# Kernel tuning notes

Measured on AMD Instinct MI355X. Metric: run time of the kernel, lower is better.

## Reference

```python
import jax, jax.numpy as jnp
import numpy as np

N_NODES = 10000
N_EDGES = 160000


def setup_inputs() -> dict:
    key = jax.random.key(0)
    ks = jax.random.split(key, 8)
    B, S, N, C, H, E = 2, 32, N_NODES, 1, 32, N_EDGES
    x = jax.random.normal(ks[0], (B, S, N, C), dtype=jnp.float32)
    mask = jax.random.randint(ks[1], (B, S, N, C), 0, 2) > 0  # True = observed
    edge_index = jax.random.randint(ks[2], (2, E), 0, N, dtype=jnp.int32)
    edge_weight = jax.random.uniform(ks[3], (E,), dtype=jnp.float32)
    W1 = jax.random.normal(ks[4], (C, H), dtype=jnp.float32) * (1.0 / np.sqrt(C))
    b1 = jnp.zeros((H,), dtype=jnp.float32)
    W2 = jax.random.normal(ks[5], (H, C), dtype=jnp.float32) * (1.0 / np.sqrt(H))
    b2 = jnp.zeros((C,), dtype=jnp.float32)
    return {"x": x, "mask": mask, "edge_index": edge_index,
            "edge_weight": edge_weight, "W1": W1, "b1": b1, "W2": W2, "b2": b2}


def _gcn_norm(edge_index, edge_weight, num_nodes, dtype):
    # PyG gcn_norm: add self-loops (weight 1), symmetric D^-1/2 A D^-1/2.
    src, dst = edge_index[0], edge_index[1]
    loop = jnp.arange(num_nodes, dtype=edge_index.dtype)
    src = jnp.concatenate([src, loop])
    dst = jnp.concatenate([dst, loop])
    w = jnp.concatenate([edge_weight, jnp.ones((num_nodes,), dtype)])
    deg = jax.ops.segment_sum(w, dst, num_segments=num_nodes)
    dinv = jnp.where(deg > 0, jax.lax.rsqrt(deg), 0.0)
    norm = dinv[src] * w * dinv[dst]  # (E + N,)
    return src, dst, norm


def _gcn_layer(h, W, b, src, dst, norm, num_nodes):
    # h: (G, N, Fin) batched over G = B*S replicas sharing one graph.
    h = h @ W                                        # (G, N, Fout)
    msg = norm[None, :, None] * h[:, src, :]         # (G, E+N, Fout)
    agg = jnp.zeros((h.shape[0], num_nodes, W.shape[1]), h.dtype)
    agg = agg.at[:, dst, :].add(msg)
    return agg + b


def reference(x, mask, edge_index, edge_weight, W1, b1, W2, b2):
    B, S, N, C = x.shape
    src, dst, norm = _gcn_norm(edge_index, edge_weight, N, x.dtype)
    h = x.reshape(B * S, N, C)  # fuse per-(batch,step) loop into one batched pass
    h = jax.nn.relu(_gcn_layer(h, W1, b1, src, dst, norm, N))
    h = _gcn_layer(h, W2, b2, src, dst, norm, N)
    out = h.reshape(B, S, N, C)
    # impute_only_holes at eval time: keep observed values
    out = jnp.where(mask, x, out)
    return out
```

## Files before the change

### kernel.cpp

```cpp
#include <hip/hip_runtime.h>


#define G   64
#define CAP 64
#define POISON   0xAAAAAAAAu
#define DEG_INV  1.52587890625e-5f

__global__ void k1_prep(const float* __restrict__ x,
                        const int* __restrict__ src, const int* __restrict__ dst,
                        const float* __restrict__ ew,
                        unsigned* __restrict__ packed,
                        int2* __restrict__ bucket, float* __restrict__ xt,
                        int N, int E, int ntile) {
    if ((int)blockIdx.x < ntile) {
        __shared__ float tile[64][65];
        int n0 = blockIdx.x * 64;
        int lane = threadIdx.x & 63, wq = threadIdx.x >> 6;
#pragma unroll
        for (int i = 0; i < 16; ++i) {
            int g = wq + i * 4;
            int n = n0 + lane;
            if (n < N) tile[g][lane] = x[(size_t)g * N + n];
        }
        __syncthreads();
#pragma unroll
        for (int i = 0; i < 16; ++i) {
            int nl = wq + i * 4;
            int n = n0 + nl;
            if (n < N) xt[(size_t)n * G + lane] = tile[lane][nl];
        }
    } else {
        int e = (blockIdx.x - ntile) * blockDim.x + threadIdx.x;
        if (e < E) {
            int d = dst[e], s = src[e];
            float w = ew[e];
            unsigned add = (1u << 24) + (unsigned)__float2uint_rn(w * 65536.0f);
            unsigned pos = (atomicAdd(&packed[d], add) >> 24) - 0xAAu;
            if (pos < CAP) bucket[(size_t)d * CAP + pos] = make_int2(s, __float_as_int(w));
        }
    }
}

__device__ __forceinline__ float di_of(unsigned hdr) {
    return rsqrtf((float)(hdr & 0xFFFFFFu) * DEG_INV + 1.0f);
}

__global__ void k2_gather_phi(const int2* __restrict__ bucket,
                              const unsigned* __restrict__ packed,
                              const float* __restrict__ xt,
                              const float* __restrict__ W1,
                              const float* __restrict__ b1,
                              const float* __restrict__ W2,
                              float* __restrict__ zt, int N) {
    int d    = (blockIdx.x * blockDim.x + threadIdx.x) >> 6;
    int lane = threadIdx.x & 63;
    if (d >= N) return;
    unsigned hdr = packed[d] - POISON;
    int kn = (int)(hdr >> 24); if (kn > CAP) kn = CAP;
    float di = di_of(hdr);
    size_t base = (size_t)d * CAP;
    const int4* b4 = (const int4*)(bucket + base);
    float sacc = 0.0f;
    int k = 0;
    for (; k + 4 <= kn; k += 4) {
        int4 pA = b4[k >> 1];
        int4 pB = b4[(k >> 1) + 1];
        float f0 = xt[(size_t)pA.x * G + lane];
        float f1 = xt[(size_t)pA.z * G + lane];
        float f2 = xt[(size_t)pB.x * G + lane];
        float f3 = xt[(size_t)pB.z * G + lane];
        unsigned h0 = packed[pA.x] - POISON;
        unsigned h1 = packed[pA.z] - POISON;
        unsigned h2 = packed[pB.x] - POISON;
        unsigned h3 = packed[pB.z] - POISON;
        sacc = fmaf(__int_as_float(pA.y) * di_of(h0), f0, sacc);
        sacc = fmaf(__int_as_float(pA.w) * di_of(h1), f1, sacc);
        sacc = fmaf(__int_as_float(pB.y) * di_of(h2), f2, sacc);
        sacc = fmaf(__int_as_float(pB.w) * di_of(h3), f3, sacc);
    }
    for (; k < kn; ++k) {
        int2 en = bucket[base + k];
        float ds = di_of(packed[en.x] - POISON);
        sacc = fmaf(__int_as_float(en.y) * ds, xt[(size_t)en.x * G + lane], sacc);
    }
    float a = fmaf(di, sacc, di * di * xt[(size_t)d * G + lane]);
    float zv = 0.0f;
#pragma unroll
    for (int f = 0; f < 32; ++f)
        zv = fmaf(fmaxf(fmaf(W1[f], a, b1[f]), 0.0f), W2[f], zv);
    zt[(size_t)d * G + lane] = di * zv;
}

__global__ void __launch_bounds__(1024)
k3_gather_fin(const int2* __restrict__ bucket,
              const unsigned* __restrict__ packed,
              const float* __restrict__ zt,
              const float* __restrict__ b2,
              const float* __restrict__ x,
              const int* __restrict__ mask,
              float* __restrict__ out, int N) {
    __shared__ float tile[16][68];
    int n0 = blockIdx.x * 16;
    int lane = threadIdx.x & 63;
    int c    = threadIdx.x >> 6;
    int d    = n0 + c;
    float b2v = b2[0];
    if (d < N) {
        unsigned hdr = packed[d] - POISON;
        int kn = (int)(hdr >> 24); if (kn > CAP) kn = CAP;
        float di = di_of(hdr);
        size_t base = (size_t)d * CAP;
        const int4* b4 = (const int4*)(bucket + base);
        float sacc = zt[(size_t)d * G + lane];
        int k = 0;
        for (; k + 4 <= kn; k += 4) {
            int4 pA = b4[k >> 1];
            int4 pB = b4[(k >> 1) + 1];
            float f0 = zt[(size_t)pA.x * G + lane];
            float f1 = zt[(size_t)pA.z * G + lane];
            float f2 = zt[(size_t)pB.x * G + lane];
            float f3 = zt[(size_t)pB.z * G + lane];
            sacc = fmaf(__int_as_float(pA.y), f0, sacc);
            sacc = fmaf(__int_as_float(pA.w), f1, sacc);
            sacc = fmaf(__int_as_float(pB.y), f2, sacc);
            sacc = fmaf(__int_as_float(pB.w), f3, sacc);
        }
        for (; k < kn; ++k) {
            int2 en = bucket[base + k];
            sacc = fmaf(__int_as_float(en.y), zt[(size_t)en.x * G + lane], sacc);
        }
        tile[c][lane] = fmaf(di, sacc, b2v);
    }
    __syncthreads();
    {
        int i = threadIdx.x;
        int g = i >> 4, cc = i & 15;
        int n = n0 + cc;
        if (n < N) {
            size_t off = (size_t)g * N + n;
            out[off] = mask[off] ? x[off] : tile[cc][g];
        }
    }
}

extern "C" void kernel_launch(void* const* d_in, const int* in_sizes, int n_in,
                              void* d_out, int out_size, void* d_ws, size_t ws_size,
                              hipStream_t stream) {
    const float* x    = (const float*)d_in[0];
    const int*   mask = (const int*)  d_in[1];
    const int*   eidx = (const int*)  d_in[2];
    const float* ew   = (const float*)d_in[3];
    const float* W1   = (const float*)d_in[4];
    const float* b1   = (const float*)d_in[5];
    const float* W2   = (const float*)d_in[6];
    const float* b2   = (const float*)d_in[7];
    float* out = (float*)d_out;

    const int E = in_sizes[3];
    const int N = in_sizes[0] / G;

    const int* src = eidx;
    const int* dst = eidx + E;

    float*    ws     = (float*)d_ws;
    unsigned* packed = (unsigned*)ws;
    int2*     bucket = (int2*)(ws + 16384);
    float*    xt     = ws + 16384 + (size_t)N * CAP * 2;
    float*    zt     = xt + (size_t)N * G;

    const int ntile = (N + 63) / 64;
    const int nscat = (E + 255) / 256;
    k1_prep<<<ntile + nscat, 256, 0, stream>>>(x, src, dst, ew, packed, bucket, xt, N, E, ntile);
    k2_gather_phi<<<(N + 3) / 4, 256, 0, stream>>>(bucket, packed, xt, W1, b1, W2, zt, N);
    k3_gather_fin<<<(N + 15) / 16, 1024, 0, stream>>>(bucket, packed, zt, b2, x, mask, out, N);
}
```

Baseline: 109.4 us.

## Split each node's gather across four edge groups with float4 loads and shuffle reduce

Both gather kernels now split each 64-lane wavefront into four 16-lane groups. Each group handles a different edge, loads 16-byte float4 vectors of node features, and the partial sums are combined with cross-lane xor shuffles. The goal is fewer serialized loop iterations per node and wider memory accesses per edge, in exchange for redundant MLP work in the three unused lane groups and extra shuffle instructions. The tail of the edge list is handled by masking invalid slots to the node itself with weight zero.

```diff
diff --git a/kernel.cpp b/kernel.cpp
--- a/kernel.cpp
+++ b/kernel.cpp
@@ -45,6 +45,14 @@
     return rsqrtf((float)(hdr & 0xFFFFFFu) * DEG_INV + 1.0f);
 }
 
+__device__ __forceinline__ float4 bfly_sum4(float4 v) {
+    v.x += __shfl_xor(v.x, 16, 64); v.y += __shfl_xor(v.y, 16, 64);
+    v.z += __shfl_xor(v.z, 16, 64); v.w += __shfl_xor(v.w, 16, 64);
+    v.x += __shfl_xor(v.x, 32, 64); v.y += __shfl_xor(v.y, 32, 64);
+    v.z += __shfl_xor(v.z, 32, 64); v.w += __shfl_xor(v.w, 32, 64);
+    return v;
+}
+
 __global__ void k2_gather_phi(const int2* __restrict__ bucket,
                               const unsigned* __restrict__ packed,
                               const float* __restrict__ xt,
@@ -55,40 +63,44 @@
     int d    = (blockIdx.x * blockDim.x + threadIdx.x) >> 6;
     int lane = threadIdx.x & 63;
     if (d >= N) return;
+    const int p = lane >> 4;
+    const int j = lane & 15;
     unsigned hdr = packed[d] - POISON;
     int kn = (int)(hdr >> 24); if (kn > CAP) kn = CAP;
     float di = di_of(hdr);
+    const float4* xt4 = (const float4*)xt;
     size_t base = (size_t)d * CAP;
-    const int4* b4 = (const int4*)(bucket + base);
-    float sacc = 0.0f;
-    int k = 0;
-    for (; k + 4 <= kn; k += 4) {
-        int4 pA = b4[k >> 1];
-        int4 pB = b4[(k >> 1) + 1];
-        float f0 = xt[(size_t)pA.x * G + lane];
-        float f1 = xt[(size_t)pA.z * G + lane];
-        float f2 = xt[(size_t)pB.x * G + lane];
-        float f3 = xt[(size_t)pB.z * G + lane];
-        unsigned h0 = packed[pA.x] - POISON;
-        unsigned h1 = packed[pA.z] - POISON;
-        unsigned h2 = packed[pB.x] - POISON;
-        unsigned h3 = packed[pB.z] - POISON;
-        sacc = fmaf(__int_as_float(pA.y) * di_of(h0), f0, sacc);
-        sacc = fmaf(__int_as_float(pA.w) * di_of(h1), f1, sacc);
-        sacc = fmaf(__int_as_float(pB.y) * di_of(h2), f2, sacc);
-        sacc = fmaf(__int_as_float(pB.w) * di_of(h3), f3, sacc);
+    float4 acc = make_float4(0.f, 0.f, 0.f, 0.f);
+    for (int k4 = 0; k4 < kn; k4 += 4) {
+        int idx = k4 + p;
+        int2 e = bucket[base + idx];
+        bool valid = idx < kn;
+        int s = valid ? e.x : d;
+        float w = valid ? __int_as_float(e.y) : 0.0f;
+        float4 v = xt4[(size_t)s * 16 + j];
+        float c = w * di_of(packed[s] - POISON);
+        acc.x = fmaf(c, v.x, acc.x); acc.y = fmaf(c, v.y, acc.y);
+        acc.z = fmaf(c, v.z, acc.z); acc.w = fmaf(c, v.w, acc.w);
     }
-    for (; k < kn; ++k) {
-        int2 en = bucket[base + k];
-        float ds = di_of(packed[en.x] - POISON);
-        sacc = fmaf(__int_as_float(en.y) * ds, xt[(size_t)en.x * G + lane], sacc);
+    acc = bfly_sum4(acc);
+    float4 xv = xt4[(size_t)d * 16 + j];
+    float dd = di * di;
+    float4 a;
+    a.x = fmaf(di, acc.x, dd * xv.x); a.y = fmaf(di, acc.y, dd * xv.y);
+    a.z = fmaf(di, acc.z, dd * xv.z); a.w = fmaf(di, acc.w, dd * xv.w);
+    float4 zv = make_float4(0.f, 0.f, 0.f, 0.f);
+#pragma unroll
+    for (int f = 0; f < 32; ++f) {
+        float w1 = W1[f], bb = b1[f], w2 = W2[f];
+        zv.x = fmaf(fmaxf(fmaf(w1, a.x, bb), 0.0f), w2, zv.x);
+        zv.y = fmaf(fmaxf(fmaf(w1, a.y, bb), 0.0f), w2, zv.y);
+        zv.z = fmaf(fmaxf(fmaf(w1, a.z, bb), 0.0f), w2, zv.z);
+        zv.w = fmaf(fmaxf(fmaf(w1, a.w, bb), 0.0f), w2, zv.w);
     }
-    float a = fmaf(di, sacc, di * di * xt[(size_t)d * G + lane]);
-    float zv = 0.0f;
-#pragma unroll
-    for (int f = 0; f < 32; ++f)
-        zv = fmaf(fmaxf(fmaf(W1[f], a, b1[f]), 0.0f), W2[f], zv);
-    zt[(size_t)d * G + lane] = di * zv;
+    if (p == 0) {
+        float4 o = make_float4(di * zv.x, di * zv.y, di * zv.z, di * zv.w);
+        ((float4*)zt)[(size_t)d * 16 + j] = o;
+    }
 }
 
 __global__ void __launch_bounds__(1024)
@@ -104,32 +116,34 @@
     int lane = threadIdx.x & 63;
     int c    = threadIdx.x >> 6;
     int d    = n0 + c;
+    const int p = lane >> 4;
+    const int j = lane & 15;
     float b2v = b2[0];
     if (d < N) {
         unsigned hdr = packed[d] - POISON;
         int kn = (int)(hdr >> 24); if (kn > CAP) kn = CAP;
         float di = di_of(hdr);
+        const float4* zt4 = (const float4*)zt;
         size_t base = (size_t)d * CAP;
-        const int4* b4 = (const int4*)(bucket + base);
-        float sacc = zt[(size_t)d * G + lane];
-        int k = 0;
-        for (; k + 4 <= kn; k += 4) {
-            int4 pA = b4[k >> 1];
-            int4 pB = b4[(k >> 1) + 1];
-            float f0 = zt[(size_t)pA.x * G + lane];
-            float f1 = zt[(size_t)pA.z * G + lane];
-            float f2 = zt[(size_t)pB.x * G + lane];
-            float f3 = zt[(size_t)pB.z * G + lane];
-            sacc = fmaf(__int_as_float(pA.y), f0, sacc);
-            sacc = fmaf(__int_as_float(pA.w), f1, sacc);
-            sacc = fmaf(__int_as_float(pB.y), f2, sacc);
-            sacc = fmaf(__int_as_float(pB.w), f3, sacc);
+        float4 self = zt4[(size_t)d * 16 + j];
+        float4 acc = (p == 0) ? self : make_float4(0.f, 0.f, 0.f, 0.f);
+        for (int k4 = 0; k4 < kn; k4 += 4) {
+            int idx = k4 + p;
+            int2 e = bucket[base + idx];
+            bool valid = idx < kn;
+            int s = valid ? e.x : d;
+            float w = valid ? __int_as_float(e.y) : 0.0f;
+            float4 v = zt4[(size_t)s * 16 + j];
+            acc.x = fmaf(w, v.x, acc.x); acc.y = fmaf(w, v.y, acc.y);
+            acc.z = fmaf(w, v.z, acc.z); acc.w = fmaf(w, v.w, acc.w);
         }
-        for (; k < kn; ++k) {
-            int2 en = bucket[base + k];
-            sacc = fmaf(__int_as_float(en.y), zt[(size_t)en.x * G + lane], sacc);
+        acc = bfly_sum4(acc);
+        if (p == 0) {
+            float4 o;
+            o.x = fmaf(di, acc.x, b2v); o.y = fmaf(di, acc.y, b2v);
+            o.z = fmaf(di, acc.z, b2v); o.w = fmaf(di, acc.w, b2v);
+            *(float4*)&tile[c][4 * j] = o;
         }
-        tile[c][lane] = fmaf(di, sacc, b2v);
     }
     __syncthreads();
     {
```

New measurement: 110.4 us. About the same (+0.9%).
